# Optimization experiments

Measured on AMD Instinct MI355X. Metric: run time of the kernel, lower is better.

Reference implementation:

```python
import jax, jax.numpy as jnp
import numpy as np

N, E = 40000, 640000
IN_DIM, HID, HEADS, OUT, NC, ASSIGN = 128, 16, 8, 128, 2, 100
SIGMA = 0.5
F_HID = HID * HEADS  # 128 = hidden_dim * n_heads


def _edge_softmax(logits, dst, n):
    # softmax over incoming edges of each destination node (DGL edge_softmax)
    m = jax.ops.segment_max(logits, dst, num_segments=n)
    ex = jnp.exp(logits - m[dst])
    den = jax.ops.segment_sum(ex, dst, num_segments=n)
    return ex / den[dst]


def _gat_conv(h, src, dst, W, al, ar, b):
    # DGL GATConv: fc (no bias) -> per-head additive attention -> edge softmax -> scatter-sum
    nH, D = al.shape
    feat = (h @ W).reshape(h.shape[0], nH, D)            # [N,H,D]
    el = (feat * al).sum(-1)                              # [N,H]
    er = (feat * ar).sum(-1)                              # [N,H]
    logits = jax.nn.leaky_relu(el[src] + er[dst], 0.2)    # [E,H]
    a = _edge_softmax(logits, dst, h.shape[0])            # [E,H]
    out = jax.ops.segment_sum(feat[src] * a[..., None], dst, num_segments=h.shape[0])
    return out + b                                        # [N,H,D]


def _bn(x, g, b, eps=1e-5):
    mu = x.mean(0)
    v = x.var(0)
    return g * (x - mu) * jax.lax.rsqrt(v + eps) + b


def _gat_layer(h, src, dst, W, al, ar, b, g, bt):
    x = _gat_conv(h, src, dst, W, al, ar, b).reshape(h.shape[0], -1)
    x = jax.nn.elu(_bn(x, g, bt))
    return h + x  # residual: in_dim == out_dim*heads


def _mask(x):
    # h[torch.isinf(h)] = 1e9
    return jnp.where(jnp.isinf(x), 1e9, x)


def setup_inputs():
    key = jax.random.key(0)
    ks = jax.random.split(key, 20)
    rn = lambda k, s: jax.random.normal(k, s, jnp.float32) * 0.1
    return {
        "h": jax.random.normal(ks[0], (N, IN_DIM), jnp.float32),
        "e": jax.random.normal(ks[1], (E, 4), jnp.float32),
        "src": jax.random.randint(ks[2], (E,), 0, N, jnp.int32),
        "dst": jax.random.randint(ks[3], (E,), 0, N, jnp.int32),
        "W_emb": rn(ks[4], (IN_DIM, F_HID)), "b_emb": jnp.zeros((F_HID,), jnp.float32),
        "Wg": rn(ks[5], (3, F_HID, F_HID)),
        "alg": rn(ks[6], (3, HEADS, HID)), "arg": rn(ks[7], (3, HEADS, HID)),
        "bg": jnp.zeros((3, HEADS, HID), jnp.float32),
        "gam": jnp.ones((3, F_HID), jnp.float32), "bet": jnp.zeros((3, F_HID), jnp.float32),
        "W3": rn(ks[8], (F_HID, OUT)), "al3": rn(ks[9], (1, OUT)), "ar3": rn(ks[10], (1, OUT)),
        "b3": jnp.zeros((1, OUT), jnp.float32),
        "gam3": jnp.ones((OUT,), jnp.float32), "bet3": jnp.zeros((OUT,), jnp.float32),
        "Wa": rn(ks[11], (F_HID, ASSIGN)), "ba": jnp.zeros((ASSIGN,), jnp.float32),
        "Wm1": rn(ks[12], (2 * OUT, OUT)), "bm1": jnp.zeros((OUT,), jnp.float32),
        "Wm2": rn(ks[13], (OUT, OUT // 2)), "bm2": jnp.zeros((OUT // 2,), jnp.float32),
        "Wm3": rn(ks[14], (OUT // 2, NC)), "bm3": jnp.zeros((NC,), jnp.float32),
    }


def reference(h, e, src, dst, W_emb, b_emb, Wg, alg, arg, bg, gam, bet,
              W3, al3, ar3, b3, gam3, bet3, Wa, ba,
              Wm1, bm1, Wm2, bm2, Wm3, bm3):
    del e  # edge_feat=False: forward never consumes edge features
    h = h @ W_emb + b_emb  # embedding_h (dropout p=0 -> identity)
    # layer 0: GATLayer
    h = _mask(_gat_layer(h, src, dst, Wg[0], alg[0], arg[0], bg[0], gam[0], bet[0]))
    # layer 1: biGATLayer -> (h, s): GAT update + soft assignment s with sigma mixing over coarse pool
    h_in = h
    h_fine = _gat_layer(h, src, dst, Wg[1], alg[1], arg[1], bg[1], gam[1], bet[1])
    s = jax.nn.softmax(h_in @ Wa + ba, axis=-1)            # [N, ASSIGN]
    h_coarse = s.T @ h_fine                                # [ASSIGN, F_HID]
    h = _mask(SIGMA * h_fine + (1.0 - SIGMA) * (s @ h_coarse))
    # layer 2: GATLayer
    h = _mask(_gat_layer(h, src, dst, Wg[2], alg[2], arg[2], bg[2], gam[2], bet[2]))
    # layer 3: GATLayer, 1 head, out_dim
    h = _mask(_gat_layer(h, src, dst, W3, al3, ar3, b3, gam3, bet3))
    # apply_edges: gather src/dst node feats, concat, MLPReadout (256->128->64->NC), inf-mask
    z = jnp.concatenate([h[src], h[dst]], axis=1)          # [E, 2*OUT]
    z = jax.nn.relu(z @ Wm1 + bm1)
    z = jax.nn.relu(z @ Wm2 + bm2)
    z = _mask(z @ Wm3 + bm3)
    return z, s
```

## Files before the change

### kernel.cpp

```cpp
#include <hip/hip_runtime.h>
#include <hip/hip_bf16.h>
#include <math.h>

#define N_ 40000
#define E_ 640000
#define CB_ 400
#define CR_ 100
#define SB_ 256
#define SNB_ 157
#define AGGB_ 2048

typedef short bf16x8 __attribute__((ext_vector_type(8)));
typedef float floatx4 __attribute__((ext_vector_type(4)));

__device__ __forceinline__ short f2bf(float f) {
    __hip_bfloat16 h = __float2bfloat16(f);
    return *reinterpret_cast<short*>(&h);
}
__device__ __forceinline__ float bf2f(short u) {
    unsigned int x = ((unsigned int)(unsigned short)u) << 16;
    return __int_as_float(x);
}
__device__ __forceinline__ float rdlane(float v, int l) {
    return __int_as_float(__builtin_amdgcn_readlane(__float_as_int(v), l));
}
__device__ __forceinline__ float bflo(unsigned int u) { return __int_as_float(u << 16); }
__device__ __forceinline__ float bfhi(unsigned int u) { return __int_as_float(u & 0xffff0000u); }

__global__ void k_count(const int* __restrict__ dst, int* __restrict__ counts) {
    for (int e = blockIdx.x * blockDim.x + threadIdx.x; e < E_; e += gridDim.x * blockDim.x)
        atomicAdd(&counts[dst[e]], 1);
}

__global__ __launch_bounds__(256) void k_scanA(const int* __restrict__ counts,
                                               int* __restrict__ excl,
                                               int* __restrict__ bsum) {
    int t = threadIdx.x;
    int i = blockIdx.x * SB_ + t;
    int v = (i < N_) ? counts[i] : 0;
    int lane = t & 63, wv = t >> 6;
    int x = v;
#pragma unroll
    for (int off = 1; off < 64; off <<= 1) {
        int y = __shfl_up(x, off);
        if (lane >= off) x += y;
    }
    __shared__ int wsum[4];
    __shared__ int woff[4];
    if (lane == 63) wsum[wv] = x;
    __syncthreads();
    if (t == 0) {
        int a = 0;
#pragma unroll
        for (int j = 0; j < 4; j++) { int tv = wsum[j]; woff[j] = a; a += tv; }
        bsum[blockIdx.x] = a;
    }
    __syncthreads();
    if (i < N_) excl[i] = x - v + woff[wv];
}

__global__ __launch_bounds__(256) void k_scanB(int* __restrict__ bsum) {
    int t = threadIdx.x;
    int v = (t < SNB_) ? bsum[t] : 0;
    int lane = t & 63, wv = t >> 6;
    int x = v;
#pragma unroll
    for (int off = 1; off < 64; off <<= 1) {
        int y = __shfl_up(x, off);
        if (lane >= off) x += y;
    }
    __shared__ int wsum[4];
    __shared__ int woff[4];
    if (lane == 63) wsum[wv] = x;
    __syncthreads();
    if (t == 0) {
        int a = 0;
#pragma unroll
        for (int j = 0; j < 4; j++) { int tv = wsum[j]; woff[j] = a; a += tv; }
    }
    __syncthreads();
    if (t < SNB_) bsum[t] = x - v + woff[wv];
}

__global__ __launch_bounds__(256) void k_scanC(const int* __restrict__ excl,
                                               const int* __restrict__ bsum,
                                               int* __restrict__ rowptr,
                                               int* __restrict__ cursor) {
    int i = blockIdx.x * 256 + threadIdx.x;
    if (i < N_) {
        int r = excl[i] + bsum[i / SB_];
        rowptr[i] = r;
        cursor[i] = r;
    }
    if (i == N_) rowptr[N_] = E_;
}

__global__ void k_fill(const int* __restrict__ src, const int* __restrict__ dst,
                       int* __restrict__ cursor, int* __restrict__ srcv,
                       unsigned short* __restrict__ dstv, int* __restrict__ eidv) {
    for (int e = blockIdx.x * blockDim.x + threadIdx.x; e < E_; e += gridDim.x * blockDim.x) {
        int d = dst[e];
        int pos = atomicAdd(&cursor[d], 1);
        srcv[pos] = src[e];
        dstv[pos] = (unsigned short)d;
        eidv[pos] = e;
    }
}

__global__ __launch_bounds__(256) void k_prep_all(const float* __restrict__ Wg,
                                                  const float* __restrict__ W3,
                                                  const float* __restrict__ Wm1,
                                                  short* __restrict__ WbT6) {
    int i = blockIdx.x * 256 + threadIdx.x;
    if (i >= 6 * 16384) return;
    int m = i >> 14;
    int r = i & 16383;
    int n = r >> 7, k = r & 127;
    const float* srcp;
    switch (m) {
        case 0: srcp = Wg; break;
        case 1: srcp = Wg + 16384; break;
        case 2: srcp = Wg + 32768; break;
        case 3: srcp = W3; break;
        case 4: srcp = Wm1; break;
        default: srcp = Wm1 + 16384; break;
    }
    WbT6[m * 16384 + n * 128 + k] = f2bf(srcp[k * 128 + n]);
}

__global__ __launch_bounds__(256) void k_prep_wela(const float* __restrict__ Wg,
                                                   const float* __restrict__ alg,
                                                   const float* __restrict__ arg_,
                                                   const float* __restrict__ W3,
                                                   const float* __restrict__ al3,
                                                   const float* __restrict__ ar3,
                                                   short* __restrict__ WelT) {
    int i = blockIdx.x * 256 + threadIdx.x;
    if (i >= 4 * 2048) return;
    int layer = i >> 11;
    int r = i & 2047;
    int n = r >> 7, k = r & 127;
    float val = 0.f;
    if (layer < 3) {
        const float* W = Wg + layer * 16384;
        const float* a = (n < 8 ? alg : arg_) + layer * 128;
        int h = n & 7;
#pragma unroll
        for (int d = 0; d < 16; d++)
            val += W[k * 128 + h * 16 + d] * a[h * 16 + d];
    } else {
        if (n == 0) { for (int c = 0; c < 128; c++) val += W3[k * 128 + c] * al3[c]; }
        else if (n == 1) { for (int c = 0; c < 128; c++) val += W3[k * 128 + c] * ar3[c]; }
    }
    WelT[layer * 2048 + n * 128 + k] = f2bf(val);
}

__global__ __launch_bounds__(256) void k_prep_hilo(const float* __restrict__ W_emb,
                                                   const float* __restrict__ Wa,
                                                   short* __restrict__ WembT_hi,
                                                   short* __restrict__ WembT_lo,
                                                   short* __restrict__ WaT_hi,
                                                   short* __restrict__ WaT_lo) {
    int i = blockIdx.x * 256 + threadIdx.x;
    if (i >= 2 * 16384) return;
    int m = i >> 14;
    int r = i & 16383;
    int n = r >> 7, k = r & 127;
    if (m == 0) {
        float w = W_emb[k * 128 + n];
        short h = f2bf(w);
        WembT_hi[n * 128 + k] = h;
        WembT_lo[n * 128 + k] = f2bf(w - bf2f(h));
    } else {
        float w = (n < 100) ? Wa[k * 100 + n] : 0.f;
        short h = f2bf(w);
        WaT_hi[n * 128 + k] = h;
        WaT_lo[n * 128 + k] = f2bf(w - bf2f(h));
    }
}

__global__ __launch_bounds__(256) void k_mfma_hilo(const float* __restrict__ A,
                                                   const short* __restrict__ BT_hi,
                                                   const short* __restrict__ BT_lo,
                                                   const float* __restrict__ bias,
                                                   float* __restrict__ C, int ncols) {
    __shared__ short sAh[64 * 136];
    __shared__ short sAl[64 * 136];
    __shared__ short sBh[128 * 136];
    int t = threadIdx.x;
    int r0 = blockIdx.x * 64;
    {
        int n = t >> 1;
        int k0 = (t & 1) * 64;
#pragma unroll
        for (int j = 0; j < 8; j++) {
            bf16x8 v = *(const bf16x8*)(BT_hi + n * 128 + k0 + 8 * j);
            *(bf16x8*)(sBh + n * 136 + k0 + 8 * j) = v;
        }
    }
    {
        int r = t >> 2;
        int k0 = (t & 3) * 32;
        const float* ar = A + (size_t)(r0 + r) * 128 + k0;
#pragma unroll
        for (int j = 0; j < 4; j++) {
            float4 f0 = *(const float4*)(ar + 8 * j);
            float4 f1 = *(const float4*)(ar + 8 * j + 4);
            float x[8] = {f0.x, f0.y, f0.z, f0.w, f1.x, f1.y, f1.z, f1.w};
            bf16x8 vh, vl;
#pragma unroll
            for (int q = 0; q < 8; q++) {
                short hh = f2bf(x[q]);
                vh[q] = hh;
                vl[q] = f2bf(x[q] - bf2f(hh));
            }
            *(bf16x8*)(sAh + r * 136 + k0 + 8 * j) = vh;
            *(bf16x8*)(sAl + r * 136 + k0 + 8 * j) = vl;
        }
    }
    __syncthreads();
    int lane = t & 63, wv = t >> 6;
    int lm = lane & 15, quad = lane >> 4;
    int m0 = wv * 16;
    bf16x8 aH[4], aL[4];
#pragma unroll
    for (int kt = 0; kt < 4; kt++) {
        aH[kt] = *(const bf16x8*)(sAh + (m0 + lm) * 136 + kt * 32 + quad * 8);
        aL[kt] = *(const bf16x8*)(sAl + (m0 + lm) * 136 + kt * 32 + quad * 8);
    }
#pragma unroll
    for (int nt = 0; nt < 8; nt++) {
        const short* blp = BT_lo + (nt * 16 + lm) * 128 + quad * 8;
        floatx4 acc = (floatx4){0.f, 0.f, 0.f, 0.f};
#pragma unroll
        for (int kt = 0; kt < 4; kt++) {
            bf16x8 bH = *(const bf16x8*)(sBh + (nt * 16 + lm) * 136 + kt * 32 + quad * 8);
            bf16x8 bL = *(const bf16x8*)(blp + kt * 32);
            acc = __builtin_amdgcn_mfma_f32_16x16x32_bf16(aH[kt], bH, acc, 0, 0, 0);
            acc = __builtin_amdgcn_mfma_f32_16x16x32_bf16(aL[kt], bH, acc, 0, 0, 0);
            acc = __builtin_amdgcn_mfma_f32_16x16x32_bf16(aH[kt], bL, acc, 0, 0, 0);
        }
        int col = nt * 16 + lm;
        if (col < ncols) {
            float bv = bias ? bias[col] : 0.f;
#pragma unroll
            for (int r = 0; r < 4; r++) {
                int row = r0 + m0 + quad * 4 + r;
                C[(size_t)row * ncols + col] = acc[r] + bv;
            }
        }
    }
}

__global__ __launch_bounds__(256) void k_gemm_mfma(const float* __restrict__ A,
                                                   const short* __restrict__ WbT,
                                                   const float* __restrict__ bias,
                                                   short* __restrict__ C,
                                                   const short* __restrict__ WelT,
                                                   float* __restrict__ el,
                                                   float* __restrict__ er,
                                                   int H,
                                                   const float* __restrict__ bnx,
                                                   const float* __restrict__ bnh,
                                                   const float* __restrict__ csum,
                                                   const float* __restrict__ csq,
                                                   const float* __restrict__ bng,
                                                   const float* __restrict__ bnb,
                                                   float* __restrict__ hout,
                                                   int do_mask,
                                                   const short* __restrict__ WbT2,
                                                   short* __restrict__ C2) {
    __shared__ short sA[64 * 136];
    __shared__ short sB[128 * 136];
    __shared__ float sScale[128];
    __shared__ float sShift[128];
    int t = threadIdx.x;
    int r0 = blockIdx.x * 64;
    if (bnx) {
        if (t < 128) {
            const float invN = 1.f / (float)N_;
            float mu = csum[t] * invN;
            float var = csq[t] * invN - mu * mu;
            float inv = rsqrtf(var + 1e-5f);
            float sc = bng[t] * inv;
            sScale[t] = sc;
            sShift[t] = bnb[t] - mu * sc;
        }
        __syncthreads();
    }
    {
        int n = t >> 1;
        int k0 = (t & 1) * 64;
#pragma unroll
        for (int j = 0; j < 8; j++) {
            bf16x8 v = *(const bf16x8*)(WbT + n * 128 + k0 + 8 * j);
            *(bf16x8*)(sB + n * 136 + k0 + 8 * j) = v;
        }
    }
    {
        int r = t >> 2;
        int k0 = (t & 3) * 32;
        if (bnx) {
            const float* xr = bnx + (size_t)(r0 + r) * 128 + k0;
            const float* hr = bnh + (size_t)(r0 + r) * 128 + k0;
            float* ho = hout + (size_t)(r0 + r) * 128 + k0;
#pragma unroll
            for (int j = 0; j < 4; j++) {
                float4 x0 = *(const float4*)(xr + 8 * j);
                float4 x1 = *(const float4*)(xr + 8 * j + 4);
                float4 h0 = *(const float4*)(hr + 8 * j);
                float4 h1 = *(const float4*)(hr + 8 * j + 4);
                float xs[8] = {x0.x, x0.y, x0.z, x0.w, x1.x, x1.y, x1.z, x1.w};
                float hs[8] = {h0.x, h0.y, h0.z, h0.w, h1.x, h1.y, h1.z, h1.w};
                float ov[8];
                bf16x8 v;
#pragma unroll
                for (int q = 0; q < 8; q++) {
                    int c = k0 + 8 * j + q;
                    float y = sScale[c] * xs[q] + sShift[c];
                    y = y > 0.f ? y : (__expf(y) - 1.f);
                    float hv = hs[q] + y;
                    if (do_mask && isinf(hv)) hv = 1e9f;
                    ov[q] = hv;
                    v[q] = f2bf(hv);
                }
                *(float4*)(ho + 8 * j) = make_float4(ov[0], ov[1], ov[2], ov[3]);
                *(float4*)(ho + 8 * j + 4) = make_float4(ov[4], ov[5], ov[6], ov[7]);
                *(bf16x8*)(sA + r * 136 + k0 + 8 * j) = v;
            }
        } else {
            const float* ar = A + (size_t)(r0 + r) * 128 + k0;
#pragma unroll
            for (int j = 0; j < 4; j++) {
                float4 f0 = *(const float4*)(ar + 8 * j);
                float4 f1 = *(const float4*)(ar + 8 * j + 4);
                bf16x8 v;
                v[0] = f2bf(f0.x); v[1] = f2bf(f0.y); v[2] = f2bf(f0.z); v[3] = f2bf(f0.w);
                v[4] = f2bf(f1.x); v[5] = f2bf(f1.y); v[6] = f2bf(f1.z); v[7] = f2bf(f1.w);
                *(bf16x8*)(sA + r * 136 + k0 + 8 * j) = v;
            }
        }
    }
    __syncthreads();
    int lane = t & 63, wv = t >> 6;
    int lm = lane & 15, quad = lane >> 4;
    int m0 = wv * 16;
    bf16x8 aF[4];
#pragma unroll
    for (int kt = 0; kt < 4; kt++)
        aF[kt] = *(const bf16x8*)(sA + (m0 + lm) * 136 + kt * 32 + quad * 8);
#pragma unroll
    for (int nt = 0; nt < 8; nt++) {
        floatx4 acc = (floatx4){0.f, 0.f, 0.f, 0.f};
#pragma unroll
        for (int kt = 0; kt < 4; kt++) {
            bf16x8 bF = *(const bf16x8*)(sB + (nt * 16 + lm) * 136 + kt * 32 + quad * 8);
            acc = __builtin_amdgcn_mfma_f32_16x16x32_bf16(aF[kt], bF, acc, 0, 0, 0);
        }
        int col = nt * 16 + lm;
        float bv = bias ? bias[col] : 0.f;
#pragma unroll
        for (int r = 0; r < 4; r++) {
            int row = r0 + m0 + quad * 4 + r;
            C[(size_t)row * 128 + col] = f2bf(acc[r] + bv);
        }
    }
    if (WelT) {
        floatx4 acc = (floatx4){0.f, 0.f, 0.f, 0.f};
#pragma unroll
        for (int kt = 0; kt < 4; kt++) {
            bf16x8 wF = *(const bf16x8*)(WelT + lm * 128 + kt * 32 + quad * 8);
            acc = __builtin_amdgcn_mfma_f32_16x16x32_bf16(aF[kt], wF, acc, 0, 0, 0);
        }
        if (H == 8) {
#pragma unroll
            for (int r = 0; r < 4; r++) {
                int row = r0 + m0 + quad * 4 + r;
                if (lm < 8) el[(size_t)row * 8 + lm] = acc[r];
                else        er[(size_t)row * 8 + (lm - 8)] = acc[r];
            }
        } else {
#pragma unroll
            for (int r = 0; r < 4; r++) {
                int row = r0 + m0 + quad * 4 + r;
                if (lm == 0) el[row] = acc[r];
                if (lm == 1) er[row] = acc[r];
            }
        }
    }
    if (WbT2) {
        __syncthreads();
        {
            int n = t >> 1;
            int k0 = (t & 1) * 64;
#pragma unroll
            for (int j = 0; j < 8; j++) {
                bf16x8 v = *(const bf16x8*)(WbT2 + n * 128 + k0 + 8 * j);
                *(bf16x8*)(sB + n * 136 + k0 + 8 * j) = v;
            }
        }
        __syncthreads();
#pragma unroll
        for (int nt = 0; nt < 8; nt++) {
            floatx4 acc = (floatx4){0.f, 0.f, 0.f, 0.f};
#pragma unroll
            for (int kt = 0; kt < 4; kt++) {
                bf16x8 bF = *(const bf16x8*)(sB + (nt * 16 + lm) * 136 + kt * 32 + quad * 8);
                acc = __builtin_amdgcn_mfma_f32_16x16x32_bf16(aF[kt], bF, acc, 0, 0, 0);
            }
            int col = nt * 16 + lm;
#pragma unroll
            for (int r = 0; r < 4; r++) {
                int row = r0 + m0 + quad * 4 + r;
                C2[(size_t)row * 128 + col] = f2bf(acc[r]);
            }
        }
    }
}

__global__ __launch_bounds__(256) void k_smax100(const float* __restrict__ logits,
                                                 float* __restrict__ s) {
    int lane = threadIdx.x & 63;
    int n = blockIdx.x * 4 + (threadIdx.x >> 6);
    if (n >= N_) return;
    bool act = lane < 50;
    float2 v = make_float2(-INFINITY, -INFINITY);
    if (act) v = *(const float2*)(logits + (size_t)n * 100 + 2 * lane);
    float mx = fmaxf(v.x, v.y);
#pragma unroll
    for (int off = 1; off < 64; off <<= 1) mx = fmaxf(mx, __shfl_xor(mx, off));
    float e0 = act ? __expf(v.x - mx) : 0.f;
    float e1 = act ? __expf(v.y - mx) : 0.f;
    float sm = e0 + e1;
#pragma unroll
    for (int off = 1; off < 64; off <<= 1) sm += __shfl_xor(sm, off);
    float inv = 1.f / sm;
    if (act) *(float2*)(s + (size_t)n * 100 + 2 * lane) = make_float2(e0 * inv, e1 * inv);
}

template <int H>
__global__ __launch_bounds__(256) void k_gat_agg(const short* __restrict__ feat,
                                                 const float* __restrict__ el,
                                                 const float* __restrict__ er,
                                                 const int* __restrict__ rowptr,
                                                 const int* __restrict__ srcv,
                                                 const float* __restrict__ bias,
                                                 float* __restrict__ xout,
                                                 float* __restrict__ psum,
                                                 float* __restrict__ psq) {
    int t = threadIdx.x;
    int lane = t & 63;
    int gw = (blockIdx.x * blockDim.x + t) >> 6;
    int nw = (gridDim.x * blockDim.x) >> 6;
    int h = lane & (H - 1);
    int f0 = 2 * lane;
    int hf = (H == 8) ? (lane >> 3) : 0;

    float stx = 0.f, sty = 0.f, qtx = 0.f, qty = 0.f;

    for (int n = gw; n < N_; n += nw) {
        int beg = rowptr[n], end = rowptr[n + 1];
        if (beg == end) {
            float2 b2 = *(const float2*)(bias + f0);
            *(float2*)(xout + (size_t)n * 128 + f0) = b2;
            stx += b2.x; sty += b2.y;
            qtx += b2.x * b2.x; qty += b2.y * b2.y;
            continue;
        }
        float ern = er[(size_t)n * H + h];
        int endm1 = end - 1;
        float m = -INFINITY, ss = 0.f;
        float accx = 0.f, accy = 0.f;
        for (int e0 = beg; e0 < end; e0 += 16) {
            int le = lane >> 3;
            int eLA = e0 + le, eLB = e0 + 8 + le;
            int eCA = eLA <= endm1 ? eLA : endm1;
            int eCB = eLB <= endm1 ? eLB : endm1;
            int sLA = srcv[eCA];
            int sLB = srcv[eCB];
            float xA = el[(size_t)sLA * H + h] + ern;
            float xB = el[(size_t)sLB * H + h] + ern;
            float lrA = xA > 0.f ? xA : 0.2f * xA;
            float lrB = xB > 0.f ? xB : 0.2f * xB;
            if (eLA > endm1) lrA = -INFINITY;
            if (eLB > endm1) lrB = -INFINITY;
            bool haveB = (e0 + 8) < end;
            unsigned int uuA[8], uuB[8];
#pragma unroll
            for (int j = 0; j < 8; j++) {
                int sj = __builtin_amdgcn_readlane(sLA, j * 8);
                uuA[j] = *(const unsigned int*)(feat + (size_t)sj * 128 + f0);
            }
            if (haveB) {
#pragma unroll
                for (int j = 0; j < 8; j++) {
                    int sj = __builtin_amdgcn_readlane(sLB, j * 8);
                    uuB[j] = *(const unsigned int*)(feat + (size_t)sj * 128 + f0);
                }
            }
#pragma unroll
            for (int j = 0; j < 8; j++) {
                float lj;
                if (H == 8) lj = __shfl(lrA, j * 8 + hf);
                else        lj = rdlane(lrA, j * 8);
                if (lj > m) {
                    float r = __expf(m - lj);
                    accx *= r; accy *= r; ss *= r; m = lj;
                }
                float w = __expf(lj - m);
                accx += w * bflo(uuA[j]);
                accy += w * bfhi(uuA[j]);
                ss += w;
            }
            if (haveB) {
#pragma unroll
                for (int j = 0; j < 8; j++) {
                    float lj;
                    if (H == 8) lj = __shfl(lrB, j * 8 + hf);
                    else        lj = rdlane(lrB, j * 8);
                    if (lj > m) {
                        float r = __expf(m - lj);
                        accx *= r; accy *= r; ss *= r; m = lj;
                    }
                    float w = __expf(lj - m);
                    accx += w * bflo(uuB[j]);
                    accy += w * bfhi(uuB[j]);
                    ss += w;
                }
            }
        }
        float inv_d = 1.f / ss;
        float2 b2 = *(const float2*)(bias + f0);
        float ox = accx * inv_d + b2.x, oy = accy * inv_d + b2.y;
        *(float2*)(xout + (size_t)n * 128 + f0) = make_float2(ox, oy);
        stx += ox; sty += oy;
        qtx += ox * ox; qty += oy * oy;
    }

    __shared__ float red[4][256];
    red[0][t] = stx; red[1][t] = sty; red[2][t] = qtx; red[3][t] = qty;
    __syncthreads();
    if (t < 64) {
        float a0 = red[0][t] + red[0][t + 64] + red[0][t + 128] + red[0][t + 192];
        float a1 = red[1][t] + red[1][t + 64] + red[1][t + 128] + red[1][t + 192];
        float q0 = red[2][t] + red[2][t + 64] + red[2][t + 128] + red[2][t + 192];
        float q1 = red[3][t] + red[3][t + 64] + red[3][t + 128] + red[3][t + 192];
        *(float2*)(psum + (size_t)blockIdx.x * 128 + 2 * t) = make_float2(a0, a1);
        *(float2*)(psq + (size_t)blockIdx.x * 128 + 2 * t) = make_float2(q0, q1);
    }
}

__global__ __launch_bounds__(256) void k_stats_reduce(const float* __restrict__ psum,
                                                      const float* __restrict__ psq,
                                                      float* __restrict__ colsum,
                                                      float* __restrict__ colsq) {
    __shared__ float ls[256], lq[256];
    int t = threadIdx.x;
    int col = t & 127, half = t >> 7;
    float s = 0.f, q = 0.f;
    for (int b = blockIdx.x * 2 + half; b < AGGB_; b += gridDim.x * 2) {
        s += psum[(size_t)b * 128 + col];
        q += psq[(size_t)b * 128 + col];
    }
    ls[t] = s; lq[t] = q;
    __syncthreads();
    if (t < 128) {
        atomicAdd(&colsum[col], ls[t] + ls[t + 128]);
        atomicAdd(&colsq[col], lq[t] + lq[t + 128]);
    }
}

__global__ __launch_bounds__(512) void k_coarse_part(const float* __restrict__ s,
                                                     const float* __restrict__ xraw,
                                                     const float* __restrict__ hprev,
                                                     const float* __restrict__ csum,
                                                     const float* __restrict__ csq,
                                                     const float* __restrict__ bng,
                                                     const float* __restrict__ bnb,
                                                     float* __restrict__ part) {
    __shared__ float sSc[128], sSh[128];
    int t = threadIdx.x;
    if (t < 128) {
        const float invN = 1.f / (float)N_;
        float mu = csum[t] * invN;
        float var = csq[t] * invN - mu * mu;
        float inv = rsqrtf(var + 1e-5f);
        float sc = bng[t] * inv;
        sSc[t] = sc;
        sSh[t] = bnb[t] - mu * sc;
    }
    __syncthreads();
    int c = t & 127;
    int g = t >> 7;
    int lane = t & 63;
    float scl = sSc[c], shf = sSh[c];
    float acc[25];
#pragma unroll
    for (int a = 0; a < 25; a++) acc[a] = 0.f;
    int n0 = blockIdx.x * CR_;
    for (int n = n0; n < n0 + CR_; n += 2) {
        float y0 = scl * xraw[(size_t)n * 128 + c] + shf;
        float y1 = scl * xraw[(size_t)(n + 1) * 128 + c] + shf;
        y0 = y0 > 0.f ? y0 : (__expf(y0) - 1.f);
        y1 = y1 > 0.f ? y1 : (__expf(y1) - 1.f);
        float hv0 = hprev[(size_t)n * 128 + c] + y0;
        float hv1 = hprev[(size_t)(n + 1) * 128 + c] + y1;
        float sv0 = 0.f, sv1 = 0.f;
        if (lane < 25) {
            sv0 = s[(size_t)n * 100 + 25 * g + lane];
            sv1 = s[(size_t)(n + 1) * 100 + 25 * g + lane];
        }
#pragma unroll
        for (int a = 0; a < 25; ++a) {
            float a0 = rdlane(sv0, a);
            float a1 = rdlane(sv1, a);
            acc[a] += a0 * hv0 + a1 * hv1;
        }
    }
    float* dstp = part + (size_t)blockIdx.x * 12800 + (size_t)(25 * g) * 128 + c;
#pragma unroll
    for (int a = 0; a < 25; a++) dstp[a * 128] = acc[a];
}

__global__ __launch_bounds__(256) void k_coarse_reduce(const float* __restrict__ part,
                                                       float* __restrict__ hc) {
    int i = blockIdx.x * blockDim.x + threadIdx.x;
    if (i >= 12800) return;
    float s0 = 0.f, s1 = 0.f, s2 = 0.f, s3 = 0.f;
    for (int b = 0; b < CB_; b += 4) {
        s0 += part[(size_t)(b + 0) * 12800 + i];
        s1 += part[(size_t)(b + 1) * 12800 + i];
        s2 += part[(size_t)(b + 2) * 12800 + i];
        s3 += part[(size_t)(b + 3) * 12800 + i];
    }
    hc[i] = (s0 + s1) + (s2 + s3);
}

__global__ __launch_bounds__(256) void k_combine(const float* __restrict__ s,
                                                 const float* __restrict__ hc,
                                                 const float* __restrict__ xraw,
                                                 const float* __restrict__ csum,
                                                 const float* __restrict__ csq,
                                                 const float* __restrict__ bng,
                                                 const float* __restrict__ bnb,
                                                 float* __restrict__ hout) {
    __shared__ float ssh[16 * 100];
    __shared__ float sSc[128], sSh[128];
    int t = threadIdx.x;
    int n0 = blockIdx.x * 16;
    if (t < 128) {
        const float invN = 1.f / (float)N_;
        float mu = csum[t] * invN;
        float var = csq[t] * invN - mu * mu;
        float inv = rsqrtf(var + 1e-5f);
        float sc = bng[t] * inv;
        sSc[t] = sc;
        sSh[t] = bnb[t] - mu * sc;
    }
    for (int u = t; u < 1600; u += 256) ssh[u] = s[(size_t)n0 * 100 + u];
    __syncthreads();
    int c = t & 127, g = t >> 7;
    float scl = sSc[c], shf = sSh[c];
    float acc[8];
#pragma unroll
    for (int r = 0; r < 8; r++) acc[r] = 0.f;
    const float* hcp = hc + c;
    for (int a = 0; a < 100; a += 4) {
        float h0 = hcp[(a + 0) * 128];
        float h1 = hcp[(a + 1) * 128];
        float h2 = hcp[(a + 2) * 128];
        float h3 = hcp[(a + 3) * 128];
#pragma unroll
        for (int r = 0; r < 8; r++) {
            float4 sv = *(const float4*)(ssh + (g * 8 + r) * 100 + a);
            acc[r] += sv.x * h0 + sv.y * h1 + sv.z * h2 + sv.w * h3;
        }
    }
#pragma unroll
    for (int r = 0; r < 8; r++) {
        int row = n0 + g * 8 + r;
        float y = scl * xraw[(size_t)row * 128 + c] + shf;
        y = y > 0.f ? y : (__expf(y) - 1.f);
        float hfine = hout[(size_t)row * 128 + c] + y;
        float v = 0.5f * hfine + 0.5f * acc[r];
        if (isinf(v)) v = 1e9f;
        hout[(size_t)row * 128 + c] = v;
    }
}

__global__ __launch_bounds__(256) void k_prep_w(const float* __restrict__ Wm2,
                                                short* __restrict__ Wm2T) {
    int i = blockIdx.x * blockDim.x + threadIdx.x;
    if (i >= 64 * 128) return;
    int n = i & 63, k = i >> 6;
    Wm2T[n * 128 + k] = f2bf(Wm2[k * 64 + n]);
}

__global__ __launch_bounds__(256) void k_edge_mlp3(const short* __restrict__ Pb,
                                                   const short* __restrict__ Qb,
                                                   const int* __restrict__ srcv,
                                                   const unsigned short* __restrict__ dstv,
                                                   const int* __restrict__ eidv,
                                                   const short* __restrict__ Wm2T,
                                                   const float* __restrict__ bm2,
                                                   const float* __restrict__ Wm3,
                                                   const float* __restrict__ bm3,
                                                   float* __restrict__ zout) {
    __shared__ short sW[64 * 128];
    int t = threadIdx.x;
    for (int u = t; u < 1024; u += 256) {
        int n = u >> 4, k16 = u & 15;
        int phys = (n << 4) | (k16 ^ (n & 15));
        *(bf16x8*)(sW + phys * 8) = *(const bf16x8*)(Wm2T + n * 128 + k16 * 8);
    }
    int lane = t & 63;
    int lm = lane & 15, quad = lane >> 4;
    float bv[4], w30[4], w31[4];
#pragma unroll
    for (int nt = 0; nt < 4; nt++) {
        int n = nt * 16 + lm;
        bv[nt] = bm2[n]; w30[nt] = Wm3[2 * n]; w31[nt] = Wm3[2 * n + 1];
    }
    float b30 = bm3[0], b31 = bm3[1];
    __syncthreads();

    int gw = (blockIdx.x * blockDim.x + t) >> 6;
    int nw = (gridDim.x * blockDim.x) >> 6;

    for (int tile = gw; tile < E_ / 16; tile += nw) {
        int p0 = tile * 16;
        int sI = srcv[p0 + lm];
        int dI = (int)dstv[p0 + lm];
        const short* pr = Pb + (size_t)sI * 128 + quad * 8;
        const short* qr = Qb + (size_t)dI * 128 + quad * 8;
        uint4 pu[4], qu[4];
#pragma unroll
        for (int kt = 0; kt < 4; kt++) {
            pu[kt] = *(const uint4*)(pr + kt * 32);
            qu[kt] = *(const uint4*)(qr + kt * 32);
        }
        bf16x8 aF[4];
#pragma unroll
        for (int kt = 0; kt < 4; kt++) {
            unsigned int pv[4] = {pu[kt].x, pu[kt].y, pu[kt].z, pu[kt].w};
            unsigned int qv[4] = {qu[kt].x, qu[kt].y, qu[kt].z, qu[kt].w};
            union { uint4 u; bf16x8 v; } cv;
            unsigned int rr[4];
#pragma unroll
            for (int j = 0; j < 4; j++) {
                float fl = fmaxf(bflo(pv[j]) + bflo(qv[j]), 0.f);
                float fh = fmaxf(bfhi(pv[j]) + bfhi(qv[j]), 0.f);
                rr[j] = (unsigned int)(unsigned short)f2bf(fl) |
                        ((unsigned int)(unsigned short)f2bf(fh) << 16);
            }
            cv.u.x = rr[0]; cv.u.y = rr[1]; cv.u.z = rr[2]; cv.u.w = rr[3];
            aF[kt] = cv.v;
        }
        float pz0[4] = {0.f, 0.f, 0.f, 0.f};
        float pz1[4] = {0.f, 0.f, 0.f, 0.f};
#pragma unroll
        for (int nt = 0; nt < 4; nt++) {
            floatx4 acc = (floatx4){0.f, 0.f, 0.f, 0.f};
#pragma unroll
            for (int kt = 0; kt < 4; kt++) {
                int phys = ((nt * 16 + lm) << 4) | (((kt << 2) | quad) ^ lm);
                bf16x8 bF = *(const bf16x8*)(sW + phys * 8);
                acc = __builtin_amdgcn_mfma_f32_16x16x32_bf16(aF[kt], bF, acc, 0, 0, 0);
            }
#pragma unroll
            for (int r = 0; r < 4; r++) {
                float u = fmaxf(acc[r] + bv[nt], 0.f);
                pz0[r] += u * w30[nt];
                pz1[r] += u * w31[nt];
            }
        }
#pragma unroll
        for (int off = 1; off < 16; off <<= 1) {
#pragma unroll
            for (int r = 0; r < 4; r++) {
                pz0[r] += __shfl_xor(pz0[r], off);
                pz1[r] += __shfl_xor(pz1[r], off);
            }
        }
        if (lm < 4) {
            int eid = eidv[p0 + quad * 4 + lm];
            float z0 = pz0[lm] + b30;
            float z1 = pz1[lm] + b31;
            if (isinf(z0)) z0 = 1e9f;
            if (isinf(z1)) z1 = 1e9f;
            *(float2*)(zout + (size_t)eid * 2) = make_float2(z0, z1);
        }
    }
}

extern "C" void kernel_launch(void* const* d_in, const int* in_sizes, int n_in,
                              void* d_out, int out_size, void* d_ws, size_t ws_size,
                              hipStream_t stream) {
    const float* h_in  = (const float*)d_in[0];
    const int*   src   = (const int*)d_in[2];
    const int*   dst   = (const int*)d_in[3];
    const float* W_emb = (const float*)d_in[4];
    const float* b_emb = (const float*)d_in[5];
    const float* Wg    = (const float*)d_in[6];
    const float* alg   = (const float*)d_in[7];
    const float* arg_  = (const float*)d_in[8];
    const float* bg    = (const float*)d_in[9];
    const float* gam   = (const float*)d_in[10];
    const float* bet   = (const float*)d_in[11];
    const float* W3    = (const float*)d_in[12];
    const float* al3   = (const float*)d_in[13];
    const float* ar3   = (const float*)d_in[14];
    const float* b3    = (const float*)d_in[15];
    const float* gam3  = (const float*)d_in[16];
    const float* bet3  = (const float*)d_in[17];
    const float* Wa    = (const float*)d_in[18];
    const float* ba    = (const float*)d_in[19];
    const float* Wm1   = (const float*)d_in[20];
    const float* bm1   = (const float*)d_in[21];
    const float* Wm2   = (const float*)d_in[22];
    const float* bm2   = (const float*)d_in[23];
    const float* Wm3   = (const float*)d_in[24];
    const float* bm3   = (const float*)d_in[25];

    float* zout = (float*)d_out;
    float* sout = zout + (size_t)E_ * 2;

    float* ws = (float*)d_ws;
    size_t o = 0;
    float* h_cur = ws + o; o += (size_t)N_ * 128;
    float* xbuf  = ws + o; o += (size_t)N_ * 128;
    float* featb = ws + o; o += (size_t)N_ * 128;
    float* el    = ws + o; o += (size_t)N_ * 8;
    float* er    = ws + o; o += (size_t)N_ * 8;
    float* colsum = ws + o; o += 128;
    float* colsq  = ws + o; o += 128;
    float* hc     = ws + o; o += 100 * 128;
    float* psum   = ws + o; o += (size_t)AGGB_ * 128;
    float* psq    = ws + o; o += (size_t)AGGB_ * 128;
    short* Wm2T = (short*)(ws + o); o += (64 * 128) / 2;
    short* WbT6 = (short*)(ws + o); o += (6 * 16384) / 2;
    short* WelT = (short*)(ws + o); o += (4 * 2048) / 2;
    short* WembT_hi = (short*)(ws + o); o += 16384 / 2;
    short* WembT_lo = (short*)(ws + o); o += 16384 / 2;
    short* WaT_hi   = (short*)(ws + o); o += 16384 / 2;
    short* WaT_lo   = (short*)(ws + o); o += 16384 / 2;
    int* counts = (int*)(ws + o); o += N_;
    int* rowptr = (int*)(ws + o); o += N_ + 4;
    int* cursor = (int*)(ws + o); o += N_;
    int* srcv   = (int*)(ws + o); o += E_;
    unsigned short* dstv = (unsigned short*)(ws + o); o += E_ / 2;
    int* eidv   = (int*)(ws + o); o += E_;
    int* bsum   = (int*)(ws + o); o += SNB_ + 4;

    short* featw = (short*)featb;

    hipMemsetAsync(counts, 0, N_ * sizeof(int), stream);
    k_count<<<1024, 256, 0, stream>>>(dst, counts);
    k_scanA<<<SNB_, 256, 0, stream>>>(counts, eidv, bsum);
    k_scanB<<<1, 256, 0, stream>>>(bsum);
    k_scanC<<<SNB_ + 1, 256, 0, stream>>>(eidv, bsum, rowptr, cursor);
    k_fill<<<1024, 256, 0, stream>>>(src, dst, cursor, srcv, dstv, eidv);
    k_prep_w<<<32, 256, 0, stream>>>(Wm2, Wm2T);
    k_prep_all<<<384, 256, 0, stream>>>(Wg, W3, Wm1, WbT6);
    k_prep_wela<<<32, 256, 0, stream>>>(Wg, alg, arg_, W3, al3, ar3, WelT);
    k_prep_hilo<<<128, 256, 0, stream>>>(W_emb, Wa, WembT_hi, WembT_lo, WaT_hi, WaT_lo);

    k_mfma_hilo<<<N_ / 64, 256, 0, stream>>>(h_in, WembT_hi, WembT_lo, b_emb, h_cur, 128);

    k_gemm_mfma<<<N_ / 64, 256, 0, stream>>>(h_cur, WbT6 + 0 * 16384, nullptr, featw,
                                             WelT + 0 * 2048, el, er, 8,
                                             nullptr, nullptr, nullptr, nullptr,
                                             nullptr, nullptr, nullptr, 0,
                                             nullptr, nullptr);
    hipMemsetAsync(colsum, 0, 256 * sizeof(float), stream);
    k_gat_agg<8><<<AGGB_, 256, 0, stream>>>(featw, el, er, rowptr, srcv, bg + 0 * 128, xbuf,
                                            psum, psq);
    k_stats_reduce<<<64, 256, 0, stream>>>(psum, psq, colsum, colsq);

    k_gemm_mfma<<<N_ / 64, 256, 0, stream>>>(nullptr, WbT6 + 1 * 16384, nullptr, featw,
                                             WelT + 1 * 2048, el, er, 8,
                                             xbuf, h_cur, colsum, colsq,
                                             gam + 0 * 128, bet + 0 * 128, h_cur, 1,
                                             nullptr, nullptr);
    k_mfma_hilo<<<N_ / 64, 256, 0, stream>>>(h_cur, WaT_hi, WaT_lo, ba, xbuf, 100);
    k_smax100<<<N_ / 4, 256, 0, stream>>>(xbuf, sout);
    hipMemsetAsync(colsum, 0, 256 * sizeof(float), stream);
    k_gat_agg<8><<<AGGB_, 256, 0, stream>>>(featw, el, er, rowptr, srcv, bg + 1 * 128, xbuf,
                                            psum, psq);
    k_stats_reduce<<<64, 256, 0, stream>>>(psum, psq, colsum, colsq);
    k_coarse_part<<<CB_, 512, 0, stream>>>(sout, xbuf, h_cur, colsum, colsq,
                                           gam + 1 * 128, bet + 1 * 128, featb);
    k_coarse_reduce<<<50, 256, 0, stream>>>(featb, hc);
    k_combine<<<N_ / 16, 256, 0, stream>>>(sout, hc, xbuf, colsum, colsq,
                                           gam + 1 * 128, bet + 1 * 128, h_cur);

    k_gemm_mfma<<<N_ / 64, 256, 0, stream>>>(h_cur, WbT6 + 2 * 16384, nullptr, featw,
                                             WelT + 2 * 2048, el, er, 8,
                                             nullptr, nullptr, nullptr, nullptr,
                                             nullptr, nullptr, nullptr, 0,
                                             nullptr, nullptr);
    hipMemsetAsync(colsum, 0, 256 * sizeof(float), stream);
    k_gat_agg<8><<<AGGB_, 256, 0, stream>>>(featw, el, er, rowptr, srcv, bg + 2 * 128, xbuf,
                                            psum, psq);
    k_stats_reduce<<<64, 256, 0, stream>>>(psum, psq, colsum, colsq);

    k_gemm_mfma<<<N_ / 64, 256, 0, stream>>>(nullptr, WbT6 + 3 * 16384, nullptr, featw,
                                             WelT + 3 * 2048, el, er, 1,
                                             xbuf, h_cur, colsum, colsq,
                                             gam + 2 * 128, bet + 2 * 128, h_cur, 1,
                                             nullptr, nullptr);
    hipMemsetAsync(colsum, 0, 256 * sizeof(float), stream);
    k_gat_agg<1><<<AGGB_, 256, 0, stream>>>(featw, el, er, rowptr, srcv, b3, xbuf,
                                            psum, psq);
    k_stats_reduce<<<64, 256, 0, stream>>>(psum, psq, colsum, colsq);

    short* Pb = (short*)featb;
    short* Qb = Pb + (size_t)N_ * 128;
    k_gemm_mfma<<<N_ / 64, 256, 0, stream>>>(nullptr, WbT6 + 4 * 16384, bm1, Pb,
                                             nullptr, nullptr, nullptr, 0,
                                             xbuf, h_cur, colsum, colsq,
                                             gam3, bet3, h_cur, 1,
                                             WbT6 + 5 * 16384, Qb);
    k_edge_mlp3<<<2048, 256, 0, stream>>>(Pb, Qb, srcv, dstv, eidv, Wm2T, bm2, Wm3, bm3, zout);
}
```

Measured before the change: 722.1 us.

## Compute coarse pooling s^T h_fine with split-bf16 MFMA instead of scalar FMAs

Replaces the scalar readlane-based s^T·h_fine partial-sum kernel with an MFMA kernel. Each block stages transposed 32-node chunks of s and the BN/ELU/residual-applied features in shared memory as hi/lo bf16 pairs, then does three bf16 MFMAs per tile to keep near-fp32 accuracy. The block count drops from 400 to 250, so the reduce kernel sums fewer partials. It adds LDS staging, padding rows to 112, and split-precision error in place of exact fp32 FMAs.

```diff
diff --git a/kernel.cpp b/kernel.cpp
--- a/kernel.cpp
+++ b/kernel.cpp
@@ -4,8 +4,7 @@
 
 #define N_ 40000
 #define E_ 640000
-#define CB_ 400
-#define CR_ 100
+#define CPB_ 250
 #define SB_ 256
 #define SNB_ 157
 #define AGGB_ 2048
@@ -570,7 +569,7 @@
     }
 }
 
-__global__ __launch_bounds__(512) void k_coarse_part(const float* __restrict__ s,
+__global__ __launch_bounds__(256) void k_coarse_mfma(const float* __restrict__ s,
                                                      const float* __restrict__ xraw,
                                                      const float* __restrict__ hprev,
                                                      const float* __restrict__ csum,
@@ -579,6 +578,8 @@
                                                      const float* __restrict__ bnb,
                                                      float* __restrict__ part) {
     __shared__ float sSc[128], sSh[128];
+    __shared__ short sSTh[112 * 40], sSTl[112 * 40];
+    __shared__ short sHfh[128 * 40], sHfl[128 * 40];
     int t = threadIdx.x;
     if (t < 128) {
         const float invN = 1.f / (float)N_;
@@ -589,51 +590,94 @@
         sSc[t] = sc;
         sSh[t] = bnb[t] - mu * sc;
     }
-    __syncthreads();
-    int c = t & 127;
-    int g = t >> 7;
-    int lane = t & 63;
-    float scl = sSc[c], shf = sSh[c];
-    float acc[25];
-#pragma unroll
-    for (int a = 0; a < 25; a++) acc[a] = 0.f;
-    int n0 = blockIdx.x * CR_;
-    for (int n = n0; n < n0 + CR_; n += 2) {
-        float y0 = scl * xraw[(size_t)n * 128 + c] + shf;
-        float y1 = scl * xraw[(size_t)(n + 1) * 128 + c] + shf;
-        y0 = y0 > 0.f ? y0 : (__expf(y0) - 1.f);
-        y1 = y1 > 0.f ? y1 : (__expf(y1) - 1.f);
-        float hv0 = hprev[(size_t)n * 128 + c] + y0;
-        float hv1 = hprev[(size_t)(n + 1) * 128 + c] + y1;
-        float sv0 = 0.f, sv1 = 0.f;
-        if (lane < 25) {
-            sv0 = s[(size_t)n * 100 + 25 * g + lane];
-            sv1 = s[(size_t)(n + 1) * 100 + 25 * g + lane];
-        }
-#pragma unroll
-        for (int a = 0; a < 25; ++a) {
-            float a0 = rdlane(sv0, a);
-            float a1 = rdlane(sv1, a);
-            acc[a] += a0 * hv0 + a1 * hv1;
-        }
-    }
-    float* dstp = part + (size_t)blockIdx.x * 12800 + (size_t)(25 * g) * 128 + c;
-#pragma unroll
-    for (int a = 0; a < 25; a++) dstp[a * 128] = acc[a];
+    int lane = t & 63, wv = t >> 6;
+    int lm = lane & 15, quad = lane >> 4;
+    floatx4 acc[7][2];
+#pragma unroll
+    for (int mt = 0; mt < 7; mt++)
+#pragma unroll
+        for (int ntl = 0; ntl < 2; ntl++)
+            acc[mt][ntl] = (floatx4){0.f, 0.f, 0.f, 0.f};
+
+    for (int ch = 0; ch < 5; ++ch) {
+        int kn0 = (blockIdx.x * 5 + ch) * 32;
+        __syncthreads();
+        for (int u = t; u < 12 * 32; u += 256) {
+            int a = 100 + (u >> 5), nd = u & 31;
+            sSTh[a * 40 + nd] = 0;
+            sSTl[a * 40 + nd] = 0;
+        }
+        for (int u = t; u < 3200; u += 256) {
+            int nd = u / 100, a = u - nd * 100;
+            float v = s[(size_t)(kn0 + nd) * 100 + a];
+            short hh = f2bf(v);
+            sSTh[a * 40 + nd] = hh;
+            sSTl[a * 40 + nd] = f2bf(v - bf2f(hh));
+        }
+        {
+            int nd = t >> 3;
+            int c0 = (t & 7) * 16;
+            const float* xr = xraw + (size_t)(kn0 + nd) * 128 + c0;
+            const float* hr = hprev + (size_t)(kn0 + nd) * 128 + c0;
+#pragma unroll
+            for (int j4 = 0; j4 < 4; ++j4) {
+                float4 xv = *(const float4*)(xr + j4 * 4);
+                float4 hv4 = *(const float4*)(hr + j4 * 4);
+                float xs[4] = {xv.x, xv.y, xv.z, xv.w};
+                float hs[4] = {hv4.x, hv4.y, hv4.z, hv4.w};
+#pragma unroll
+                for (int q = 0; q < 4; ++q) {
+                    int c = c0 + j4 * 4 + q;
+                    float y = sSc[c] * xs[q] + sSh[c];
+                    y = y > 0.f ? y : (__expf(y) - 1.f);
+                    float hv = hs[q] + y;
+                    short hh = f2bf(hv);
+                    sHfh[c * 40 + nd] = hh;
+                    sHfl[c * 40 + nd] = f2bf(hv - bf2f(hh));
+                }
+            }
+        }
+        __syncthreads();
+#pragma unroll
+        for (int ntl = 0; ntl < 2; ++ntl) {
+            int n0 = (wv * 2 + ntl) * 16;
+            bf16x8 bH = *(const bf16x8*)(sHfh + (n0 + lm) * 40 + quad * 8);
+            bf16x8 bL = *(const bf16x8*)(sHfl + (n0 + lm) * 40 + quad * 8);
+#pragma unroll
+            for (int mt = 0; mt < 7; ++mt) {
+                bf16x8 aH = *(const bf16x8*)(sSTh + (mt * 16 + lm) * 40 + quad * 8);
+                bf16x8 aL = *(const bf16x8*)(sSTl + (mt * 16 + lm) * 40 + quad * 8);
+                acc[mt][ntl] = __builtin_amdgcn_mfma_f32_16x16x32_bf16(aH, bH, acc[mt][ntl], 0, 0, 0);
+                acc[mt][ntl] = __builtin_amdgcn_mfma_f32_16x16x32_bf16(aL, bH, acc[mt][ntl], 0, 0, 0);
+                acc[mt][ntl] = __builtin_amdgcn_mfma_f32_16x16x32_bf16(aH, bL, acc[mt][ntl], 0, 0, 0);
+            }
+        }
+    }
+    float* pb = part + (size_t)blockIdx.x * 12800;
+#pragma unroll
+    for (int ntl = 0; ntl < 2; ++ntl) {
+        int col = (wv * 2 + ntl) * 16 + lm;
+#pragma unroll
+        for (int mt = 0; mt < 7; ++mt) {
+#pragma unroll
+            for (int r = 0; r < 4; ++r) {
+                int row = mt * 16 + quad * 4 + r;
+                if (row < 100) pb[row * 128 + col] = acc[mt][ntl][r];
+            }
+        }
+    }
 }
 
 __global__ __launch_bounds__(256) void k_coarse_reduce(const float* __restrict__ part,
                                                        float* __restrict__ hc) {
     int i = blockIdx.x * blockDim.x + threadIdx.x;
     if (i >= 12800) return;
-    float s0 = 0.f, s1 = 0.f, s2 = 0.f, s3 = 0.f;
-    for (int b = 0; b < CB_; b += 4) {
+    float s0 = 0.f, s1 = 0.f;
+    for (int b = 0; b < CPB_; b += 2) {
         s0 += part[(size_t)(b + 0) * 12800 + i];
         s1 += part[(size_t)(b + 1) * 12800 + i];
-        s2 += part[(size_t)(b + 2) * 12800 + i];
-        s3 += part[(size_t)(b + 3) * 12800 + i];
-    }
-    hc[i] = (s0 + s1) + (s2 + s3);
+    }
+    hc[i] = s0 + s1;
 }
 
 __global__ __launch_bounds__(256) void k_combine(const float* __restrict__ s,
@@ -888,8 +932,8 @@
     k_gat_agg<8><<<AGGB_, 256, 0, stream>>>(featw, el, er, rowptr, srcv, bg + 1 * 128, xbuf,
                                             psum, psq);
     k_stats_reduce<<<64, 256, 0, stream>>>(psum, psq, colsum, colsq);
-    k_coarse_part<<<CB_, 512, 0, stream>>>(sout, xbuf, h_cur, colsum, colsq,
-                                           gam + 1 * 128, bet + 1 * 128, featb);
+    k_coarse_mfma<<<CPB_, 256, 0, stream>>>(sout, xbuf, h_cur, colsum, colsq,
+                                            gam + 1 * 128, bet + 1 * 128, featb);
     k_coarse_reduce<<<50, 256, 0, stream>>>(featb, hc);
     k_combine<<<N_ / 16, 256, 0, stream>>>(sout, hc, xbuf, colsum, colsq,
                                            gam + 1 * 128, bet + 1 * 128, h_cur);
```

Result: faster. 702.5 us (-2.7%).
